# Kernel tuning notes

Measured on AMD Instinct MI355X. Metric: run time of the kernel, lower is better.

The kernel has to match this reference:

```python
import jax, jax.numpy as jnp
import numpy as np

B, S, D = 8, 4096, 192
MEM_READ, MEM_WRITE, MEM_READY = 156, 157, 158


def setup_inputs() -> dict:
    key = jax.random.key(0)
    ks = jax.random.split(key, 9)
    inp = {"x": jax.random.normal(ks[0], (B, S, D), dtype=jnp.float32)}
    names = ["Wq_r", "Wk_r", "Wv_r", "Wo_r", "Wq_w", "Wk_w", "Wv_w", "Wo_w"]
    for i, n in enumerate(names):
        inp[n] = jax.random.normal(ks[i + 1], (D, D), dtype=jnp.float32) * 0.02
    return inp


def _attention(x, Wq, Wk, Wv, Wo):
    # single-head, non-causal PureAttention: q/k/v = x @ W.T, softmax(qk^T/sqrt(D)) v, then W_o
    q = jnp.einsum('bsd,ed->bse', x, Wq)
    k = jnp.einsum('bsd,ed->bse', x, Wk)
    v = jnp.einsum('bsd,ed->bse', x, Wv)
    scale = jnp.asarray(1.0 / np.sqrt(D), x.dtype)
    scores = jnp.einsum('bqe,bke->bqk', q, k) * scale  # [B,S,S]
    attn = jax.nn.softmax(scores, axis=-1)
    o = jnp.einsum('bqk,bke->bqe', attn, v)
    return jnp.einsum('bse,oe->bso', o, Wo)


def reference(x, Wq_r, Wk_r, Wv_r, Wo_r, Wq_w, Wk_w, Wv_w, Wo_w):
    read_flag = x[:, 0, MEM_READ]    # [B]
    write_flag = x[:, 0, MEM_WRITE]  # [B]
    read_res = _attention(x, Wq_r, Wk_r, Wv_r, Wo_r)
    write_res = _attention(x, Wq_w, Wk_w, Wv_w, Wo_w)
    rg = read_flag[:, None, None]
    wg = write_flag[:, None, None]
    out = x + rg * (read_res - x) + wg * (write_res - x)
    out = out.at[:, :, MEM_READ].set(0.0)
    out = out.at[:, :, MEM_WRITE].set(0.0)
    ready = (read_flag + write_flag)[:, None]  # broadcast over seq
    out = out.at[:, :, MEM_READY].set(jnp.broadcast_to(ready, out.shape[:2]))
    return out
```

## Files before the change

kernel.cpp:

```cpp
#include <hip/hip_runtime.h>
#include <stdint.h>

#define B_ 8
#define S_ 4096
#define D_ 192
#define M_ (B_*S_)
#define VTILE 7680
#define KTILE 6400

typedef short v8s __attribute__((ext_vector_type(8)));
typedef float v4f __attribute__((ext_vector_type(4)));
typedef unsigned long long ull;

static __device__ __forceinline__ unsigned short f2bf(float f){
  union{float f; unsigned u;} v; v.f=f;
  unsigned u = v.u;
  unsigned r = (u + 0x7fffu + ((u>>16)&1u))>>16;
  return (unsigned short)r;
}
static __device__ __forceinline__ float fexp2(float x){
  return __builtin_amdgcn_exp2f(x);
}

static __device__ __forceinline__ unsigned sw_fp8(float x){
  union{float f; unsigned u;} v; v.f = x;
  unsigned s = (v.u >> 24) & 0x80u;
  float a = fabsf(x);
  if (a < 0.001953125f) return s;
  if (a >= 240.f) return s | 0x7Eu;
  if (a < 0.015625f) {
    int m = (int)(a*512.f + 0.5f); if(m>7) m=7;
    return s | (unsigned)m;
  }
  int e = (int)((v.u >> 23) & 0xff) - 127;
  unsigned mant = (v.u >> 20) & 0x7u;
  unsigned rest = v.u & 0xFFFFFu;
  if (rest > 0x80000u || (rest == 0x80000u && (mant&1u))) mant++;
  unsigned ee = (unsigned)(e + 7);
  if (mant == 8u){ mant = 0u; ee++; }
  return s | (ee<<3) | mant;
}
template<bool HI>
static __device__ __forceinline__ unsigned pk8(float a, float b, unsigned old){
#if __has_builtin(__builtin_amdgcn_cvt_pk_fp8_f32)
  return __builtin_amdgcn_cvt_pk_fp8_f32(a, b, old, HI);
#else
  unsigned p = sw_fp8(a) | (sw_fp8(b)<<8);
  return HI ? ((old & 0x0000FFFFu) | (p<<16)) : ((old & 0xFFFF0000u) | p);
#endif
}

typedef const __attribute__((address_space(1))) unsigned int gu32;
typedef __attribute__((address_space(3))) unsigned int lu32;
#define GLL16(gp, lp) __builtin_amdgcn_global_load_lds((gu32*)(gp), (lu32*)(lp), 16, 0, 0)

__global__ void cvt_w_kernel(const float* w0,const float* w1,const float* w2,const float* w3,
                             const float* w4,const float* w5,const float* w6,const float* w7,
                             unsigned short* dst){
  int w = blockIdx.y;
  const float* src;
  switch(w){
    case 0: src=w0; break; case 1: src=w1; break; case 2: src=w2; break; case 3: src=w3; break;
    case 4: src=w4; break; case 5: src=w5; break; case 6: src=w6; break; default: src=w7; break;
  }
  int i = blockIdx.x*256 + threadIdx.x;
  float v = src[i];
  if(w==0 || w==4 || w==1 || w==5) v *= 0.32267249f;
  dst[(size_t)w*36864 + i] = f2bf(v);
}

__global__ __launch_bounds__(256) void proj_kernel(
    const float* __restrict__ x, const unsigned short* __restrict__ Wb,
    unsigned char* __restrict__ Q8g, unsigned char* __restrict__ K8t,
    unsigned char* __restrict__ V8)
{
  __shared__ __align__(16) unsigned char Vstage8[2*VTILE];
  const size_t MDB = (size_t)M_*D_;
  int path = blockIdx.y;
  int tid = threadIdx.x;
  int wid = tid>>6, lane = tid&63;
  int lr = lane&15, lg = lane>>4, kb = lg*8;
  int m0 = blockIdx.x*64 + wid*16;
  int row = m0 + lr;

  v8s a[6];
  #pragma unroll
  for(int c=0;c<6;c++){
    const float* xp = &x[(size_t)row*D_ + c*32 + kb];
    float4 f0 = *(const float4*)xp;
    float4 f1 = *(const float4*)(xp+4);
    v8s t;
    t[0]=(short)f2bf(f0.x); t[1]=(short)f2bf(f0.y); t[2]=(short)f2bf(f0.z); t[3]=(short)f2bf(f0.w);
    t[4]=(short)f2bf(f1.x); t[5]=(short)f2bf(f1.y); t[6]=(short)f2bf(f1.z); t[7]=(short)f2bf(f1.w);
    a[c]=t;
  }
  int bidx = m0 / S_;
  int sb   = (blockIdx.x*64) % S_;
  int sloc = wid*16 + lg*4;

  {
    const unsigned short* W = Wb + (size_t)(path*4 + 0)*36864;
    unsigned char* dst = Q8g + (size_t)path*MDB;
    #pragma unroll
    for(int nt=0; nt<12; nt++){
      v4f acc = {0.f,0.f,0.f,0.f};
      int n = nt*16 + lr;
      #pragma unroll
      for(int c=0;c<6;c++){
        v8s bfr = *(const v8s*)&W[(size_t)n*D_ + c*32 + kb];
        acc = __builtin_amdgcn_mfma_f32_16x16x32_bf16(a[c], bfr, acc, 0,0,0);
      }
      int col = nt*16 + lr;
      int r0 = m0 + lg*4;
      #pragma unroll
      for(int r=0;r<4;r++){
        unsigned p = pk8<false>(acc[r], 0.f, 0u);
        dst[(size_t)(r0+r)*D_ + col] = (unsigned char)(p & 0xFF);
      }
    }
  }
  {
    const unsigned short* W = Wb + (size_t)(path*4 + 1)*36864;
    unsigned char* dstK = K8t + ((size_t)path*B_ + bidx)*128*KTILE;
    #pragma unroll
    for(int nt=0; nt<12; nt++){
      v4f acc = {0.f,0.f,0.f,0.f};
      int n = nt*16 + lr;
      #pragma unroll
      for(int c=0;c<6;c++){
        v8s bfr = *(const v8s*)&W[(size_t)n*D_ + c*32 + kb];
        acc = __builtin_amdgcn_mfma_f32_16x16x32_bf16(a[c], bfr, acc, 0,0,0);
      }
      int col = nt*16 + lr;
      #pragma unroll
      for(int r=0;r<4;r++){
        int rowS = sb + sloc + r;
        unsigned p = pk8<false>(acc[r], 0.f, 0u);
        dstK[(size_t)(rowS>>5)*KTILE + (rowS&31)*200 + col] = (unsigned char)(p & 0xFF);
      }
    }
  }
  {
    const unsigned short* W = Wb + (size_t)(path*4 + 2)*36864;
    int t2 = sloc >> 5, s32 = sloc & 31;
    #pragma unroll
    for(int nt=0; nt<12; nt++){
      v4f acc = {0.f,0.f,0.f,0.f};
      int n = nt*16 + lr;
      #pragma unroll
      for(int c=0;c<6;c++){
        v8s bfr = *(const v8s*)&W[(size_t)n*D_ + c*32 + kb];
        acc = __builtin_amdgcn_mfma_f32_16x16x32_bf16(a[c], bfr, acc, 0,0,0);
      }
      int col = nt*16 + lr;
      unsigned pk4 = pk8<false>(acc[0], acc[1], 0u);
      pk4 = pk8<true>(acc[2], acc[3], pk4);
      *(unsigned*)&Vstage8[t2*VTILE + col*40 + s32] = pk4;
    }
    __syncthreads();
    unsigned char* dstV = V8 + (size_t)path*((size_t)B_*128*VTILE)
                        + ((size_t)bidx*128 + (sb>>5))*VTILE;
    #pragma unroll
    for(int j=0;j<4;j++){
      int i = tid + j*256;
      if(i<960) *(v8s*)&dstV[i*16] = *(const v8s*)&Vstage8[i*16];
    }
  }
}

#define KSTR8 200

__global__ __launch_bounds__(512,4) void attn_kernel(
    const unsigned char* __restrict__ Q8g,
    const unsigned char* __restrict__ K8t,
    const unsigned char* __restrict__ V8,
    unsigned short* __restrict__ Ob)
{
  __shared__ __align__(16) unsigned char KL[2][KTILE];
  __shared__ __align__(16) unsigned char VL8[3][VTILE];

  int flat = blockIdx.x + 32*blockIdx.y + 256*blockIdx.z;
  int w = (flat&7)*64 + (flat>>3);
  int qi = w & 31;
  int b  = (w>>5) & 7;
  int z  = w>>8;

  const size_t MDB = (size_t)M_*D_;
  const unsigned char* Q8 = Q8g + (size_t)z*MDB;
  const unsigned char* Kp = K8t + ((size_t)z*B_ + b)*128*KTILE;
  const unsigned char* Vp = V8 + (size_t)z*((size_t)B_*128*VTILE) + (size_t)b*128*VTILE;
  unsigned short* O = Ob + (size_t)z*MDB;

  int q0 = qi*128;
  int tid = threadIdx.x, wid=tid>>6, lane=tid&63;
  int lr = lane&15, lg = lane>>4;
  size_t bK = (size_t)b*S_*D_;
  int qrow0 = q0 + wid*16;

  bool doK = tid < 400;
  bool doV = tid < 480;

  long qf8[6];
  {
    const unsigned char* qp = Q8 + bK + (size_t)(qrow0 + lr)*D_;
    #pragma unroll
    for(int c=0;c<6;c++) qf8[c] = *(const long*)(qp + c*32 + lg*8);
  }
  float lsum = 0.f;
  v4f oacc[12];
  #pragma unroll
  for(int e=0;e<12;e++) oacc[e] = (v4f){0.f,0.f,0.f,0.f};

  auto stage = [&](int t, int kbuf, int vbuf){
    if(doK) GLL16(Kp + (size_t)t*KTILE + tid*16, &KL[kbuf][tid*16]);
    if(doV) GLL16(Vp + (size_t)t*VTILE + tid*16, &VL8[vbuf][tid*16]);
  };
  auto do_qk = [&](int kcur, v4f sacc[2]){
    __builtin_amdgcn_s_setprio(1);
    #pragma unroll
    for(int ct=0; ct<2; ct++){
      v4f s = {0.f,0.f,0.f,0.f};
      const unsigned char* rb = &KL[kcur][(ct*16+lr)*KSTR8];
      #pragma unroll
      for(int c=0;c<6;c++){
        long kf8 = *(const long*)(rb + c*32 + lg*8);
        s = __builtin_amdgcn_mfma_f32_16x16x32_fp8_fp8(kf8, qf8[c], s, 0,0,0);
      }
      sacc[ct]=s;
    }
    __builtin_amdgcn_s_setprio(0);
  };
  auto do_softmax = [&](v4f sacc[2], long& pa8){
    float p00=fexp2(sacc[0][0]), p01=fexp2(sacc[0][1]);
    float p02=fexp2(sacc[0][2]), p03=fexp2(sacc[0][3]);
    float p10=fexp2(sacc[1][0]), p11=fexp2(sacc[1][1]);
    float p12=fexp2(sacc[1][2]), p13=fexp2(sacc[1][3]);
    lsum += ((p00+p01)+(p02+p03)) + ((p10+p11)+(p12+p13));
    unsigned A = pk8<false>(p00,p01,0u); A = pk8<true>(p02,p03,A);
    unsigned Bx= pk8<false>(p10,p11,0u); Bx= pk8<true>(p12,p13,Bx);
    asm("v_permlane32_swap_b32 %0, %1" : "+v"(Bx), "+v"(A));
    asm("v_permlane16_swap_b32 %0, %1" : "+v"(Bx), "+v"(A));
    pa8 = (long)(((ull)Bx<<32) | (ull)A);
  };
  auto do_pv = [&](int vcur, long pa8){
    __builtin_amdgcn_s_setprio(1);
    #pragma unroll
    for(int e=0;e<12;e++){
      long vb8 = *(const long*)&VL8[vcur][(e*16+lr)*40 + lg*8];
      oacc[e] = __builtin_amdgcn_mfma_f32_16x16x32_fp8_fp8(pa8, vb8, oacc[e], 0,0,0);
    }
    __builtin_amdgcn_s_setprio(0);
  };

  stage(0, 0, 0);
  asm volatile("s_waitcnt vmcnt(0)" ::: "memory");
  __syncthreads();

  long pa_prev;
  {
    v4f sacc[2];
    do_qk(0, sacc);
    stage(1, 1, 1);
    __builtin_amdgcn_sched_barrier(0);
    do_softmax(sacc, pa_prev);
    asm volatile("s_waitcnt vmcnt(0)" ::: "memory");
    __syncthreads();
  }

  for(int t=1; t<128; t++){
    v4f sacc[2];
    do_qk(t&1, sacc);
    if(t<127) stage(t+1, (t+1)&1, (t+1)%3);
    __builtin_amdgcn_sched_barrier(0);
    do_pv((t-1)%3, pa_prev);
    do_softmax(sacc, pa_prev);
    asm volatile("s_waitcnt vmcnt(0)" ::: "memory");
    __syncthreads();
  }
  do_pv(127%3, pa_prev);

  float ps = lsum;
  ps += __shfl_xor(ps, 16);
  ps += __shfl_xor(ps, 32);
  float iv = 1.0f/ps;
  float invr[4];
  #pragma unroll
  for(int r=0;r<4;r++) invr[r] = __shfl(iv, lg*4+r, 16);
  size_t orow0 = ((size_t)b*S_ + qrow0 + lg*4)*D_;
  #pragma unroll
  for(int e=0;e<12;e++){
    #pragma unroll
    for(int r=0;r<4;r++){
      O[orow0 + (size_t)r*D_ + e*16 + lr] = f2bf(oacc[e][r]*invr[r]);
    }
  }
}

__global__ __launch_bounds__(256) void final_kernel(
  const float* __restrict__ x,
  const unsigned short* __restrict__ Or,
  const unsigned short* __restrict__ Ow,
  const unsigned short* __restrict__ WoR,
  const unsigned short* __restrict__ WoW,
  float* __restrict__ out)
{
  int halfn = blockIdx.y;
  int tid=threadIdx.x, wid=tid>>6, lane=tid&63;
  int lr=lane&15, lg=lane>>4, kb=lg*8;
  int m0 = blockIdx.x*64 + wid*16;
  int arow = m0 + lr;
  v8s ar[6], aw[6];
  #pragma unroll
  for(int c=0;c<6;c++){
    ar[c] = *(const v8s*)&Or[(size_t)arow*D_ + c*32 + kb];
    aw[c] = *(const v8s*)&Ow[(size_t)arow*D_ + c*32 + kb];
  }
  int bidx = m0 / S_;
  float rf = x[(size_t)bidx*S_*D_ + 156];
  float wf = x[(size_t)bidx*S_*D_ + 157];
  #pragma unroll
  for(int ntl=0; ntl<6; ntl++){
    int nt = halfn*6 + ntl;
    v4f accR={0.f,0.f,0.f,0.f}, accW={0.f,0.f,0.f,0.f};
    int n = nt*16 + lr;
    #pragma unroll
    for(int c=0;c<6;c++){
      v8s br = *(const v8s*)&WoR[(size_t)n*D_ + c*32 + kb];
      accR = __builtin_amdgcn_mfma_f32_16x16x32_bf16(ar[c], br, accR,0,0,0);
      v8s bw = *(const v8s*)&WoW[(size_t)n*D_ + c*32 + kb];
      accW = __builtin_amdgcn_mfma_f32_16x16x32_bf16(aw[c], bw, accW,0,0,0);
    }
    #pragma unroll
    for(int r=0;r<4;r++){
      int row = m0 + lg*4 + r;
      int col = nt*16 + lr;
      float xv = x[(size_t)row*D_ + col];
      float val = xv + rf*(accR[r]-xv) + wf*(accW[r]-xv);
      if(col==156||col==157) val = 0.f;
      else if(col==158) val = rf+wf;
      out[(size_t)row*D_ + col] = val;
    }
  }
}

extern "C" void kernel_launch(void* const* d_in, const int* in_sizes, int n_in,
                              void* d_out, int out_size, void* d_ws, size_t ws_size,
                              hipStream_t stream) {
  const float* x = (const float*)d_in[0];
  char* wsb = (char*)d_ws;
  const size_t WSZ = 36864;
  const size_t MDB = (size_t)M_*D_;
  const size_t K8SZ = (size_t)2*B_*128*KTILE;
  const size_t V8SZ = (size_t)2*B_*128*VTILE;
  unsigned short* Wb  = (unsigned short*)wsb;
  unsigned char*  Q8  = (unsigned char*)(wsb + 8*WSZ*2);
  unsigned char*  K8t = Q8 + 2*MDB;
  unsigned char*  V8  = K8t + K8SZ;
  unsigned short* Ob  = (unsigned short*)(V8 + V8SZ);

  cvt_w_kernel<<<dim3(144,8),256,0,stream>>>(
      (const float*)d_in[1],(const float*)d_in[2],(const float*)d_in[3],(const float*)d_in[4],
      (const float*)d_in[5],(const float*)d_in[6],(const float*)d_in[7],(const float*)d_in[8], Wb);

  proj_kernel<<<dim3(512,2),256,0,stream>>>(x, Wb, Q8, K8t, V8);
  attn_kernel<<<dim3(32,8,2),512,0,stream>>>(Q8, K8t, V8, Ob);
  final_kernel<<<dim3(512,2),256,0,stream>>>(x, Ob, Ob + MDB,
                                             Wb+3*WSZ, Wb+7*WSZ, (float*)d_out);
}
```

Baseline: 298.8 us.

## Double attention key tile from 32 to 64 keys per iteration

Widens each attention K/V tile to 64 keys, which halves the loop trips and halves the per-iteration barriers and waitcnt stalls. The projection kernel now writes K and V in a matching 64-key tiled layout, with a V stride of 72. Each iteration now runs four QK MFMA column tiles and two PV MFMAs per output block. LDS use per block grows, and register pressure rises from the larger score and probability arrays, which may lower occupancy under the 4-blocks launch bound.

```diff
diff --git a/kernel.cpp b/kernel.cpp
--- a/kernel.cpp
+++ b/kernel.cpp
@@ -5,8 +5,9 @@
 #define S_ 4096
 #define D_ 192
 #define M_ (B_*S_)
-#define VTILE 7680
-#define KTILE 6400
+#define VTILE 13824
+#define KTILE 12800
+#define NT_ 64
 
 typedef short v8s __attribute__((ext_vector_type(8)));
 typedef float v4f __attribute__((ext_vector_type(4)));
@@ -74,7 +75,7 @@
     unsigned char* __restrict__ Q8g, unsigned char* __restrict__ K8t,
     unsigned char* __restrict__ V8)
 {
-  __shared__ __align__(16) unsigned char Vstage8[2*VTILE];
+  __shared__ __align__(16) unsigned char Vstage8[VTILE];
   const size_t MDB = (size_t)M_*D_;
   int path = blockIdx.y;
   int tid = threadIdx.x;
@@ -96,6 +97,7 @@
   }
   int bidx = m0 / S_;
   int sb   = (blockIdx.x*64) % S_;
+  int tile = sb >> 6;
   int sloc = wid*16 + lg*4;
 
   {
@@ -121,7 +123,7 @@
   }
   {
     const unsigned short* W = Wb + (size_t)(path*4 + 1)*36864;
-    unsigned char* dstK = K8t + ((size_t)path*B_ + bidx)*128*KTILE;
+    unsigned char* dstK = K8t + (((size_t)path*B_ + bidx)*NT_ + tile)*KTILE;
     #pragma unroll
     for(int nt=0; nt<12; nt++){
       v4f acc = {0.f,0.f,0.f,0.f};
@@ -134,15 +136,13 @@
       int col = nt*16 + lr;
       #pragma unroll
       for(int r=0;r<4;r++){
-        int rowS = sb + sloc + r;
         unsigned p = pk8<false>(acc[r], 0.f, 0u);
-        dstK[(size_t)(rowS>>5)*KTILE + (rowS&31)*200 + col] = (unsigned char)(p & 0xFF);
+        dstK[(size_t)(sloc+r)*200 + col] = (unsigned char)(p & 0xFF);
       }
     }
   }
   {
     const unsigned short* W = Wb + (size_t)(path*4 + 2)*36864;
-    int t2 = sloc >> 5, s32 = sloc & 31;
     #pragma unroll
     for(int nt=0; nt<12; nt++){
       v4f acc = {0.f,0.f,0.f,0.f};
@@ -155,20 +155,17 @@
       int col = nt*16 + lr;
       unsigned pk4 = pk8<false>(acc[0], acc[1], 0u);
       pk4 = pk8<true>(acc[2], acc[3], pk4);
-      *(unsigned*)&Vstage8[t2*VTILE + col*40 + s32] = pk4;
+      *(unsigned*)&Vstage8[col*72 + sloc] = pk4;
     }
     __syncthreads();
-    unsigned char* dstV = V8 + (size_t)path*((size_t)B_*128*VTILE)
-                        + ((size_t)bidx*128 + (sb>>5))*VTILE;
+    unsigned char* dstV = V8 + (((size_t)path*B_ + bidx)*NT_ + tile)*VTILE;
     #pragma unroll
     for(int j=0;j<4;j++){
       int i = tid + j*256;
-      if(i<960) *(v8s*)&dstV[i*16] = *(const v8s*)&Vstage8[i*16];
-    }
-  }
-}
-
-#define KSTR8 200
+      if(i<864) *(v8s*)&dstV[i*16] = *(const v8s*)&Vstage8[i*16];
+    }
+  }
+}
 
 __global__ __launch_bounds__(512,4) void attn_kernel(
     const unsigned char* __restrict__ Q8g,
@@ -187,8 +184,8 @@
 
   const size_t MDB = (size_t)M_*D_;
   const unsigned char* Q8 = Q8g + (size_t)z*MDB;
-  const unsigned char* Kp = K8t + ((size_t)z*B_ + b)*128*KTILE;
-  const unsigned char* Vp = V8 + (size_t)z*((size_t)B_*128*VTILE) + (size_t)b*128*VTILE;
+  const unsigned char* Kp = K8t + ((size_t)z*B_ + b)*NT_*KTILE;
+  const unsigned char* Vp = V8 + ((size_t)z*B_ + b)*NT_*VTILE;
   unsigned short* O = Ob + (size_t)z*MDB;
 
   int q0 = qi*128;
@@ -197,9 +194,6 @@
   size_t bK = (size_t)b*S_*D_;
   int qrow0 = q0 + wid*16;
 
-  bool doK = tid < 400;
-  bool doV = tid < 480;
-
   long qf8[6];
   {
     const unsigned char* qp = Q8 + bK + (size_t)(qrow0 + lr)*D_;
@@ -211,16 +205,23 @@
   #pragma unroll
   for(int e=0;e<12;e++) oacc[e] = (v4f){0.f,0.f,0.f,0.f};
 
+  bool k2 = tid < 288;
+  bool v2 = tid < 352;
+
   auto stage = [&](int t, int kbuf, int vbuf){
-    if(doK) GLL16(Kp + (size_t)t*KTILE + tid*16, &KL[kbuf][tid*16]);
-    if(doV) GLL16(Vp + (size_t)t*VTILE + tid*16, &VL8[vbuf][tid*16]);
+    const unsigned char* kg = Kp + (size_t)t*KTILE;
+    const unsigned char* vg = Vp + (size_t)t*VTILE;
+    GLL16(kg + tid*16, &KL[kbuf][tid*16]);
+    if(k2) GLL16(kg + (512+tid)*16, &KL[kbuf][(512+tid)*16]);
+    GLL16(vg + tid*16, &VL8[vbuf][tid*16]);
+    if(v2) GLL16(vg + (512+tid)*16, &VL8[vbuf][(512+tid)*16]);
   };
-  auto do_qk = [&](int kcur, v4f sacc[2]){
+  auto do_qk = [&](int kcur, v4f sacc[4]){
     __builtin_amdgcn_s_setprio(1);
     #pragma unroll
-    for(int ct=0; ct<2; ct++){
+    for(int ct=0; ct<4; ct++){
       v4f s = {0.f,0.f,0.f,0.f};
-      const unsigned char* rb = &KL[kcur][(ct*16+lr)*KSTR8];
+      const unsigned char* rb = &KL[kcur][(ct*16+lr)*200];
       #pragma unroll
       for(int c=0;c<6;c++){
         long kf8 = *(const long*)(rb + c*32 + lg*8);
@@ -230,24 +231,29 @@
     }
     __builtin_amdgcn_s_setprio(0);
   };
-  auto do_softmax = [&](v4f sacc[2], long& pa8){
-    float p00=fexp2(sacc[0][0]), p01=fexp2(sacc[0][1]);
-    float p02=fexp2(sacc[0][2]), p03=fexp2(sacc[0][3]);
-    float p10=fexp2(sacc[1][0]), p11=fexp2(sacc[1][1]);
-    float p12=fexp2(sacc[1][2]), p13=fexp2(sacc[1][3]);
-    lsum += ((p00+p01)+(p02+p03)) + ((p10+p11)+(p12+p13));
-    unsigned A = pk8<false>(p00,p01,0u); A = pk8<true>(p02,p03,A);
-    unsigned Bx= pk8<false>(p10,p11,0u); Bx= pk8<true>(p12,p13,Bx);
-    asm("v_permlane32_swap_b32 %0, %1" : "+v"(Bx), "+v"(A));
-    asm("v_permlane16_swap_b32 %0, %1" : "+v"(Bx), "+v"(A));
-    pa8 = (long)(((ull)Bx<<32) | (ull)A);
+  auto do_softmax = [&](v4f sacc[4], long pa8[2]){
+    #pragma unroll
+    for(int h=0; h<2; h++){
+      v4f s0 = sacc[2*h], s1 = sacc[2*h+1];
+      float p00=fexp2(s0[0]), p01=fexp2(s0[1]), p02=fexp2(s0[2]), p03=fexp2(s0[3]);
+      float p10=fexp2(s1[0]), p11=fexp2(s1[1]), p12=fexp2(s1[2]), p13=fexp2(s1[3]);
+      lsum += ((p00+p01)+(p02+p03)) + ((p10+p11)+(p12+p13));
+      unsigned A = pk8<false>(p00,p01,0u); A = pk8<true>(p02,p03,A);
+      unsigned Bx= pk8<false>(p10,p11,0u); Bx= pk8<true>(p12,p13,Bx);
+      asm("v_permlane32_swap_b32 %0, %1" : "+v"(Bx), "+v"(A));
+      asm("v_permlane16_swap_b32 %0, %1" : "+v"(Bx), "+v"(A));
+      pa8[h] = (long)(((ull)Bx<<32) | (ull)A);
+    }
   };
-  auto do_pv = [&](int vcur, long pa8){
+  auto do_pv = [&](int vcur, long pa8[2]){
     __builtin_amdgcn_s_setprio(1);
     #pragma unroll
     for(int e=0;e<12;e++){
-      long vb8 = *(const long*)&VL8[vcur][(e*16+lr)*40 + lg*8];
-      oacc[e] = __builtin_amdgcn_mfma_f32_16x16x32_fp8_fp8(pa8, vb8, oacc[e], 0,0,0);
+      const unsigned char* vr = &VL8[vcur][(e*16+lr)*72 + lg*8];
+      long vb0 = *(const long*)(vr);
+      long vb1 = *(const long*)(vr + 32);
+      oacc[e] = __builtin_amdgcn_mfma_f32_16x16x32_fp8_fp8(pa8[0], vb0, oacc[e], 0,0,0);
+      oacc[e] = __builtin_amdgcn_mfma_f32_16x16x32_fp8_fp8(pa8[1], vb1, oacc[e], 0,0,0);
     }
     __builtin_amdgcn_s_setprio(0);
   };
@@ -256,9 +262,9 @@
   asm volatile("s_waitcnt vmcnt(0)" ::: "memory");
   __syncthreads();
 
-  long pa_prev;
-  {
-    v4f sacc[2];
+  long pa_prev[2];
+  {
+    v4f sacc[4];
     do_qk(0, sacc);
     stage(1, 1, 1);
     __builtin_amdgcn_sched_barrier(0);
@@ -267,17 +273,17 @@
     __syncthreads();
   }
 
-  for(int t=1; t<128; t++){
-    v4f sacc[2];
+  for(int t=1; t<NT_; t++){
+    v4f sacc[4];
     do_qk(t&1, sacc);
-    if(t<127) stage(t+1, (t+1)&1, (t+1)%3);
+    if(t<NT_-1) stage(t+1, (t+1)&1, (t+1)%3);
     __builtin_amdgcn_sched_barrier(0);
     do_pv((t-1)%3, pa_prev);
     do_softmax(sacc, pa_prev);
     asm volatile("s_waitcnt vmcnt(0)" ::: "memory");
     __syncthreads();
   }
-  do_pv(127%3, pa_prev);
+  do_pv((NT_-1)%3, pa_prev);
 
   float ps = lsum;
   ps += __shfl_xor(ps, 16);
@@ -350,8 +356,8 @@
   char* wsb = (char*)d_ws;
   const size_t WSZ = 36864;
   const size_t MDB = (size_t)M_*D_;
-  const size_t K8SZ = (size_t)2*B_*128*KTILE;
-  const size_t V8SZ = (size_t)2*B_*128*VTILE;
+  const size_t K8SZ = (size_t)2*B_*NT_*KTILE;
+  const size_t V8SZ = (size_t)2*B_*NT_*VTILE;
   unsigned short* Wb  = (unsigned short*)wsb;
   unsigned char*  Q8  = (unsigned char*)(wsb + 8*WSZ*2);
   unsigned char*  K8t = Q8 + 2*MDB;
```

New measurement: 288.5 us. -3.4%, faster.
